# Performance work log

Hardware: AMD Instinct MI355X
Metric: run time of the kernel (lower is better)

## Reference

```python
import jax, jax.numpy as jnp
import numpy as np

H = 768; P = 128; HEADS = 12; LAYERS = 3; T = 17; VD = 10
D = H // HEADS
H2 = H // 2


def _ln(x, s, b, eps=1e-5):
    m = x.mean(-1, keepdims=True)
    v = ((x - m) ** 2).mean(-1, keepdims=True)
    return (x - m) * jax.lax.rsqrt(v + eps) * s + b


def _gru_dir(x, wih, whh, bih, bhh, reverse):
    # torch nn.GRU single direction, batch_first
    if reverse:
        x = x[:, ::-1]
    xw = x @ wih.T + bih  # [B,N,3*H2]
    def step(h, xw_t):
        gh = h @ whh.T + bhh
        ir, iz, inn = jnp.split(xw_t, 3, -1)
        hr, hz, hn = jnp.split(gh, 3, -1)
        r = jax.nn.sigmoid(ir + hr)
        z = jax.nn.sigmoid(iz + hz)
        n = jnp.tanh(inn + r * hn)
        h = (1.0 - z) * n + z * h
        return h, h
    h0 = jnp.zeros((x.shape[0], whh.shape[1]), x.dtype)
    _, ys = jax.lax.scan(step, h0, jnp.swapaxes(xw, 0, 1))
    ys = jnp.swapaxes(ys, 0, 1)
    return ys[:, ::-1] if reverse else ys


def setup_inputs():
    B, EDU = 2, 95
    N = EDU + 1
    key = jax.random.key(0)
    ks = iter(jax.random.split(key, 64))
    def nrm(shape, s=0.02):
        return s * jax.random.normal(next(ks), shape, jnp.float32)
    inp = {}
    inp['sentences'] = jax.random.normal(next(ks), (B, EDU, H), jnp.float32)
    inp['speakers'] = jax.random.randint(next(ks), (B, N, N), 0, 2)
    inp['turns'] = jax.random.randint(next(ks), (B, N, N), 0, 2)
    g = jax.random.randint(next(ks), (B, N, N), 0, T)
    inp['graphs'] = jnp.tril(g, -1)  # gold graph: lower-triangular relation labels
    inp['edu_nums'] = jax.random.randint(next(ks), (B,), 60, N + 1)
    inp['root'] = jnp.zeros((H,), jnp.float32)
    for d_ in ['f', 'b']:
        inp[f'gru_wih_{d_}'] = nrm((3 * H2, H))
        inp[f'gru_whh_{d_}'] = nrm((3 * H2, H2))
        inp[f'gru_bih_{d_}'] = jnp.zeros((3 * H2,), jnp.float32)
        inp[f'gru_bhh_{d_}'] = jnp.zeros((3 * H2,), jnp.float32)
    inp['emb_speaker'] = nrm((2, P // 4), 1.0)
    inp['emb_turn'] = nrm((2, P // 4), 1.0)
    inp['emb_position'] = nrm((2 * VD + 3, P // 2), 1.0)
    inp['normal_type'] = nrm((T - 1, P), P ** -0.5)
    inp['wr'] = nrm((P, 2 * H + P)); inp['br'] = jnp.zeros((P,), jnp.float32)
    inp['wz'] = nrm((P, 2 * H + P)); inp['bz'] = jnp.zeros((P,), jnp.float32)
    inp['wc'] = nrm((P, 2 * H)); inp['bc'] = jnp.zeros((P,), jnp.float32)
    inp['wu'] = nrm((P, P)); inp['bu'] = jnp.zeros((P,), jnp.float32)
    for nm in ['wq', 'wk', 'wv', 'wo']:
        inp[nm] = nrm((H, H))
    for nm in ['bq', 'bk', 'bv', 'bo']:
        inp[nm] = jnp.zeros((H,), jnp.float32)
    inp['wsk'] = nrm((D, P)); inp['bsk'] = jnp.zeros((D,), jnp.float32)
    inp['wsv'] = nrm((D, P)); inp['bsv'] = jnp.zeros((D,), jnp.float32)
    inp['ln_s'] = jnp.ones((H,), jnp.float32); inp['ln_b'] = jnp.zeros((H,), jnp.float32)
    inp['pln_s'] = jnp.ones((P,), jnp.float32); inp['pln_b'] = jnp.zeros((P,), jnp.float32)
    CIN = 4 * H + P
    inp['link_w1'] = nrm((H, CIN)); inp['link_b1'] = jnp.zeros((H,), jnp.float32)
    inp['link_w2'] = nrm((1, H)); inp['link_b2'] = jnp.zeros((1,), jnp.float32)
    inp['lab_w1'] = nrm((H, CIN)); inp['lab_b1'] = jnp.zeros((H,), jnp.float32)
    inp['lab_w2'] = nrm((T, H)); inp['lab_b2'] = jnp.zeros((T,), jnp.float32)
    return inp


def reference(sentences, speakers, turns, graphs, edu_nums, root,
              gru_wih_f, gru_whh_f, gru_bih_f, gru_bhh_f,
              gru_wih_b, gru_whh_b, gru_bih_b, gru_bhh_b,
              emb_speaker, emb_turn, emb_position, normal_type,
              wr, br, wz, bz, wc, bc, wu, bu,
              wq, bq, wk, bk, wv, bv, wo, bo, wsk, bsk, wsv, bsv,
              ln_s, ln_b, pln_s, pln_b,
              link_w1, link_b1, link_w2, link_b2,
              lab_w1, lab_b1, lab_w2, lab_b2):
    B, EDU, _ = sentences.shape
    N = EDU + 1
    # root node + EDU embeddings -> bidirectional dialog GRU
    dialog_input = jnp.concatenate([jnp.broadcast_to(root, (B, 1, H)), sentences], axis=1)
    fw = _gru_dir(dialog_input, gru_wih_f, gru_whh_f, gru_bih_f, gru_bhh_f, False)
    bw = _gru_dir(dialog_input, gru_wih_b, gru_whh_b, gru_bih_b, gru_bhh_b, True)
    dialog_output = jnp.concatenate([fw, bw], -1)  # [B,N,H]
    # attention masking bias
    valid = jnp.arange(N)[None, :] < edu_nums[:, None]
    bias = jnp.where(valid, 0.0, -1e9)[:, None, None, :]  # [B,1,1,N]
    # constant path embedding (speaker / turn / relative position)
    idx = jnp.arange(N)
    rel = jnp.clip(idx[None, :] - idx[:, None], -VD - 1, VD + 1) + VD + 1
    pos = jnp.broadcast_to(emb_position[rel][None], (B, N, N, P // 2))
    const_path = jnp.concatenate([emb_speaker[speakers], emb_turn[turns], pos], -1)
    # gold structure path from relation labels (PathModel, padding_idx=0)
    labels = jnp.concatenate([jnp.zeros((1, P), normal_type.dtype), normal_type], 0)
    struct_path = labels[graphs + jnp.swapaxes(graphs, 1, 2)]  # [B,N,N,P]
    tril = jnp.tril(jnp.ones((N, N), bool), -1)
    triu = jnp.triu(jnp.ones((N, N), bool), 1)
    nodes = dialog_output
    scale = D ** -0.5
    for _ in range(LAYERS):
        # dns2ds: symmetrize (in-place in torch, so struct_path is replaced)
        struct_path = jnp.where(triu[None, :, :, None], jnp.swapaxes(struct_path, 1, 2), struct_path)
        paths = _ln(struct_path + const_path, pln_s, pln_b)
        q = (nodes @ wq.T + bq).reshape(B, N, HEADS, D).transpose(0, 2, 1, 3) * scale
        k = (nodes @ wk.T + bk).reshape(B, N, HEADS, D).transpose(0, 2, 1, 3)
        v = (nodes @ wv.T + bv).reshape(B, N, HEADS, D).transpose(0, 2, 1, 3)
        sk = paths @ wsk.T + bsk  # [B,N,N,D]
        sv = paths @ wsv.T + bsv
        w = (jnp.einsum('bhnd,bhmd->bhnm', q, k)
             + jnp.einsum('bhnd,bnmd->bhnm', q, sk) + bias)
        w = jax.nn.softmax(w, -1)
        out = (jnp.einsum('bhnm,bhmd->bhnd', w, v)
               + jnp.einsum('bhnm,bnmd->bhnd', w, sv))
        out = out.transpose(0, 2, 1, 3).reshape(B, N, H)
        nodes = _ln(nodes + jax.nn.relu(out @ wo.T + bo), ln_s, ln_b)
        # PathUpdateModel (GRU-style update on lower-triangular pairs)
        a = jnp.broadcast_to(nodes[:, None, :, :], (B, N, N, H))  # a[b,i,j]=nodes[b,j]
        pair = jnp.concatenate([a, jnp.swapaxes(a, 1, 2)], -1)  # [B,N,N,2H]
        rz = jnp.concatenate([pair, struct_path], -1)
        r = jax.nn.sigmoid(rz @ wr.T + br)
        z = jax.nn.sigmoid(rz @ wz.T + bz)
        u = jnp.tanh(pair @ wc.T + bc + r * (struct_path @ wu.T + bu))
        new = z * struct_path + (1.0 - z) * u
        struct_path = jnp.where(tril[None, :, :, None], new, struct_path)
    # pairwise classifier features
    multi = jnp.concatenate([dialog_input, dialog_output], -1)  # [B,N,2H]
    e = jnp.broadcast_to(multi[:, None, :, :], (B, N, N, 2 * H))
    feats = jnp.concatenate([e, jnp.swapaxes(e, 1, 2), struct_path], -1)  # [B,N,N,4H+P]
    link = (jnp.tanh(feats @ link_w1.T + link_b1) @ link_w2.T + link_b2)[..., 0]
    label = jnp.tanh(feats @ lab_w1.T + lab_b1) @ lab_w2.T + lab_b2
    return (link, label)
```

## Files before the change

kernel.cpp:

```cpp
#include <hip/hip_runtime.h>
#include <math.h>

typedef unsigned short u16;
typedef short bf16x8 __attribute__((ext_vector_type(8)));
typedef float f32x4 __attribute__((ext_vector_type(4)));


static constexpr size_t O_MULTI  = 0;
static constexpr size_t O_XWF    = O_MULTI + 294912;
static constexpr size_t O_XWB    = O_XWF   + 221184;
static constexpr size_t O_HBUF   = O_XWB   + 221184;
static constexpr size_t O_CONST  = O_HBUF  + 3072;
static constexpr size_t O_STRUCT = O_CONST + 2359296;
static constexpr size_t O_PATHS  = O_STRUCT+ 2359296;
static constexpr size_t O_NODES  = O_PATHS + 2359296;
static constexpr size_t O_QB     = O_NODES + 147456;
static constexpr size_t O_KB     = O_QB    + 147456;
static constexpr size_t O_VB     = O_KB    + 147456;
static constexpr size_t O_SKB    = O_VB    + 147456;
static constexpr size_t O_SVB    = O_SKB   + 1179648;
static constexpr size_t O_ATT    = O_SVB   + 1179648;
static constexpr size_t O_NP     = O_ATT   + 147456;
static constexpr size_t O_LAL    = O_NP    + 147456;
static constexpr size_t O_LBL    = O_LAL   + 147456;
static constexpr size_t O_LAB    = O_LBL   + 147456;
static constexpr size_t O_LBB    = O_LAB   + 147456;
static constexpr size_t O_END    = O_LBB   + 147456;

static constexpr int B_QW  = 0;
static constexpr int B_KW  = 589824;
static constexpr int B_VW  = 1179648;
static constexpr int B_OW  = 1769472;
static constexpr int B_IHF = 2359296;
static constexpr int B_IHB = 3244032;
static constexpr int B_RA  = 4128768;
static constexpr int B_RB  = 4227072;
static constexpr int B_ZA  = 4325376;
static constexpr int B_ZB  = 4423680;
static constexpr int B_CA  = 4521984;
static constexpr int B_CB  = 4620288;
static constexpr int B_CBF = 4718592;
static constexpr int B_MBF = 4980736;
static constexpr int B_NBF = 5275648;
static constexpr int B_ABF = 5423104;
static constexpr int B_TOT = 5570560;
static constexpr int CVT_TOT = 4980736;

static constexpr int C_WSK = 0;
static constexpr int C_WSV = 8192;
static constexpr int C_WRS = 16384;
static constexpr int C_WZS = 32768;
static constexpr int C_WU  = 49152;
static constexpr int C_W1L = 65536;
static constexpr int C_W1B = 163840;

__device__ __forceinline__ u16 f2bf(float f) {
  union { float f; unsigned u; } v; v.f = f;
  unsigned r = v.u + 0x7fff + ((v.u >> 16) & 1);
  return (u16)(r >> 16);
}

__global__ void init_kernel(const float* __restrict__ sentences,
                            const float* __restrict__ root,
                            float* __restrict__ multi, u16* __restrict__ multibf,
                            int* bar) {
  int idx = blockIdx.x * 256 + threadIdx.x;
  if (idx < 12) bar[idx * 64] = 0;
  if (idx >= 2 * 96 * 768) return;
  int c = idx % 768;
  int rem = idx / 768;
  int t = rem % 96;
  int b = rem / 96;
  float v = (t == 0) ? root[c] : sentences[((size_t)(b * 95 + (t - 1))) * 768 + c];
  size_t a = ((size_t)(b * 96 + t)) * 1536 + c;
  multi[a] = v;
  multibf[a] = f2bf(v);
}

__global__ void init_pairs_kernel(const int* __restrict__ speakers,
                                  const int* __restrict__ turns,
                                  const int* __restrict__ graphs,
                                  const float* __restrict__ emb_speaker,
                                  const float* __restrict__ emb_turn,
                                  const float* __restrict__ emb_position,
                                  const float* __restrict__ normal_type,
                                  float* __restrict__ cpath,
                                  float* __restrict__ spath) {
  int idx = blockIdx.x * 256 + threadIdx.x;
  if (idx >= 18432 * 128) return;
  int c = idx & 127;
  int p = idx >> 7;
  int j = p % 96;
  int rem = p / 96;
  int i = rem % 96;
  int b = rem / 96;
  float cv;
  if (c < 32) {
    cv = emb_speaker[speakers[p] * 32 + c];
  } else if (c < 64) {
    cv = emb_turn[turns[p] * 32 + (c - 32)];
  } else {
    int d = j - i;
    d = min(max(d, -11), 11) + 11;
    cv = emb_position[d * 64 + (c - 64)];
  }
  cpath[idx] = cv;
  int g2 = graphs[p] + graphs[(b * 96 + j) * 96 + i];
  spath[idx] = (g2 == 0) ? 0.f : normal_type[(g2 - 1) * 128 + c];
}

__global__ void cvt_weights_kernel(const float* __restrict__ wq, const float* __restrict__ wk,
                                   const float* __restrict__ wv, const float* __restrict__ wo,
                                   const float* __restrict__ wih_f, const float* __restrict__ wih_b,
                                   const float* __restrict__ wr, const float* __restrict__ wz,
                                   const float* __restrict__ wc, const float* __restrict__ wsk,
                                   const float* __restrict__ wsv, const float* __restrict__ wu,
                                   const float* __restrict__ link_w1, const float* __restrict__ lab_w1,
                                   u16* __restrict__ wbf) {
  int idx = blockIdx.x * 256 + threadIdx.x;
  if (idx >= CVT_TOT) return;
  float v;
  if (idx < B_IHF) {
    int which = idx / 589824, r = idx % 589824;
    const float* src = which == 0 ? wq : which == 1 ? wk : which == 2 ? wv : wo;
    v = src[r];
  } else if (idx < B_RA) {
    int r = idx - B_IHF;
    v = (r < 884736) ? wih_f[r] : wih_b[r - 884736];
  } else if (idx < B_CBF) {
    int r = idx - B_RA;
    int seg = r / 98304, q = r % 98304;
    int row = q / 768, c = q % 768;
    switch (seg) {
      case 0: v = wr[(size_t)row * 1664 + c]; break;
      case 1: v = wr[(size_t)row * 1664 + 768 + c]; break;
      case 2: v = wz[(size_t)row * 1664 + c]; break;
      case 3: v = wz[(size_t)row * 1664 + 768 + c]; break;
      case 4: v = wc[(size_t)row * 1536 + c]; break;
      default: v = wc[(size_t)row * 1536 + 768 + c]; break;
    }
  } else {
    int r = idx - B_CBF;
    if (r < C_WSV) v = wsk[r];
    else if (r < C_WRS) v = wsv[r - C_WSV];
    else if (r < C_WZS) { int q = r - C_WRS; v = wr[(size_t)(q >> 7) * 1664 + 1536 + (q & 127)]; }
    else if (r < C_WU)  { int q = r - C_WZS; v = wz[(size_t)(q >> 7) * 1664 + 1536 + (q & 127)]; }
    else if (r < C_W1L) v = wu[r - C_WU];
    else if (r < C_W1B) { int q = r - C_W1L; v = link_w1[(size_t)(q >> 7) * 3200 + 3072 + (q & 127)]; }
    else { int q = r - C_W1B; v = lab_w1[(size_t)(q >> 7) * 3200 + 3072 + (q & 127)]; }
  }
  wbf[idx] = f2bf(v);
}

__global__ void cvt_w1ab_kernel(const float* __restrict__ link_w1,
                                const float* __restrict__ lab_w1,
                                u16* __restrict__ l1, u16* __restrict__ b1) {
  int idx = blockIdx.x * 256 + threadIdx.x;
  if (idx >= 2359296) return;
  int half = idx / 1179648;
  int r = idx % 1179648;
  int row = r / 1536, c = r % 1536;
  size_t src = (size_t)row * 3200 + half * 1536 + c;
  l1[idx] = f2bf(link_w1[src]);
  b1[idx] = f2bf(lab_w1[src]);
}

struct BJob { const u16* W; const float* bias; float* C; };
struct BJobs { BJob j[6]; };

__global__ __launch_bounds__(256) void bgemm_kernel(const u16* __restrict__ A,
                                                    int lda, int K, int N, BJobs jobs) {
  BJob jb = jobs.j[blockIdx.z];
  int r0 = blockIdx.x * 16;
  int tid = threadIdx.x;
  int wave = tid >> 6, lane = tid & 63;
  int col = lane & 15, quad = lane >> 4;
  int c = blockIdx.y * 64 + wave * 16 + col;
  const u16* arow = A + (size_t)(r0 + col) * lda + quad * 8;
  const u16* brow = jb.W + (size_t)c * K + quad * 8;
  f32x4 acc = {0.f, 0.f, 0.f, 0.f};
  for (int k = 0; k < K; k += 32) {
    bf16x8 af = *(const bf16x8*)(arow + k);
    bf16x8 bf = *(const bf16x8*)(brow + k);
    acc = __builtin_amdgcn_mfma_f32_16x16x32_bf16(af, bf, acc, 0, 0, 0);
  }
  float bv = jb.bias ? jb.bias[c] : 0.f;
#pragma unroll
  for (int r = 0; r < 4; ++r)
    jb.C[(size_t)(r0 + quad * 4 + r) * N + c] = acc[r] + bv;
}

__global__ __launch_bounds__(512) void gru_kernel(const float* __restrict__ whh_f,
                                                  const float* __restrict__ whh_b,
                                                  const float* __restrict__ bhh_f,
                                                  const float* __restrict__ bhh_b,
                                                  const float* __restrict__ xwf,
                                                  const float* __restrict__ xwb,
                                                  float* hbuf, float* multi,
                                                  u16* multibf, int* bar) {
  int dir = blockIdx.x / 6;
  int sub = blockIdx.x % 6;
  const float* whh = dir ? whh_b : whh_f;
  const float* bhh = dir ? bhh_b : bhh_f;
  const float* xw = dir ? xwb : xwf;
  float* hb = hbuf + (size_t)dir * 1536;
  int* flags = bar + dir * 6 * 64;

  __shared__ float hlds[768];
  __shared__ float part[3][64][2][17];

  int tid = threadIdx.x;
  int ks = tid >> 5;
  int ug = tid & 31;
  int hv0 = ug * 2;

  float4 wreg[6][6];
#pragma unroll
  for (int d = 0; d < 2; ++d)
#pragma unroll
    for (int g = 0; g < 3; ++g) {
      const float* wrow = whh + (size_t)(g * 384 + sub * 64 + hv0 + d) * 384 + ks * 24;
#pragma unroll
      for (int m = 0; m < 6; ++m) wreg[d * 3 + g][m] = *(const float4*)(wrow + m * 4);
    }
  float bh0 = 0.f, bh1 = 0.f, bh2 = 0.f;
  int hvC = 0, bsel = 0;
  if (tid < 128) {
    hvC = sub * 64 + (tid >> 1);
    bsel = tid & 1;
    bh0 = bhh[hvC];
    bh1 = bhh[384 + hvC];
    bh2 = bhh[768 + hvC];
  }

  for (int s = 0; s < 96; ++s) {
    int t = dir ? (95 - s) : s;
    float xr = 0.f, xz = 0.f, xn = 0.f;
    if (tid < 128) {
      const float* xrow = xw + (size_t)(bsel * 96 + t) * 1152;
      xr = xrow[hvC]; xz = xrow[384 + hvC]; xn = xrow[768 + hvC];
    }
    if (s == 0) {
      __syncthreads();
      for (int k = tid; k < 768; k += 512) hlds[k] = 0.f;
    } else {
      if (tid < 6) {
        while (__hip_atomic_load(&flags[tid * 64], __ATOMIC_RELAXED,
                                 __HIP_MEMORY_SCOPE_AGENT) < s)
          __builtin_amdgcn_s_sleep(1);
      }
      __syncthreads();
      const float* hsrc = hb + ((s - 1) & 1) * 768;
      for (int k = tid; k < 768; k += 512)
        hlds[k] = __hip_atomic_load(&hsrc[k], __ATOMIC_RELAXED, __HIP_MEMORY_SCOPE_AGENT);
    }
    __syncthreads();

    float acc[6][2];
#pragma unroll
    for (int b = 0; b < 2; ++b) {
      float4 h4[6];
      const float* hp = hlds + b * 384 + ks * 24;
#pragma unroll
      for (int m = 0; m < 6; ++m) h4[m] = *(const float4*)(hp + m * 4);
#pragma unroll
      for (int u = 0; u < 6; ++u) {
        float ssum = 0.f;
#pragma unroll
        for (int m = 0; m < 6; ++m) {
          float4 w = wreg[u][m];
          ssum += w.x * h4[m].x + w.y * h4[m].y + w.z * h4[m].z + w.w * h4[m].w;
        }
        acc[u][b] = ssum;
      }
    }
#pragma unroll
    for (int d = 0; d < 2; ++d)
#pragma unroll
      for (int g = 0; g < 3; ++g) {
        part[g][hv0 + d][0][ks] = acc[d * 3 + g][0];
        part[g][hv0 + d][1][ks] = acc[d * 3 + g][1];
      }
    __syncthreads();

    float hn = 0.f;
    if (tid < 128) {
      int hv = tid >> 1;
      float gr = bh0, gz = bh1, gn = bh2;
#pragma unroll
      for (int q = 0; q < 16; ++q) {
        gr += part[0][hv][bsel][q];
        gz += part[1][hv][bsel][q];
        gn += part[2][hv][bsel][q];
      }
      float r = 1.f / (1.f + expf(-(xr + gr)));
      float z = 1.f / (1.f + expf(-(xz + gz)));
      float n = tanhf(xn + r * gn);
      float hp = hlds[bsel * 384 + hvC];
      hn = (1.f - z) * n + z * hp;
      __hip_atomic_store(&hb[(s & 1) * 768 + bsel * 384 + hvC], hn, __ATOMIC_RELAXED,
                         __HIP_MEMORY_SCOPE_AGENT);
    }
    asm volatile("s_waitcnt vmcnt(0)" ::: "memory");
    __syncthreads();
    if (tid == 0)
      __hip_atomic_store(&flags[sub * 64], s + 1, __ATOMIC_RELAXED,
                         __HIP_MEMORY_SCOPE_AGENT);
    if (tid < 128) {
      size_t a = ((size_t)(bsel * 96 + t)) * 1536 + 768 + dir * 384 + hvC;
      multi[a] = hn;
      multibf[a] = f2bf(hn);
    }
  }
}

__global__ __launch_bounds__(256) void ln_paths_kernel(float* __restrict__ spath,
                                                       const float* __restrict__ cpath,
                                                       const float* __restrict__ pln_s,
                                                       const float* __restrict__ pln_b,
                                                       u16* __restrict__ paths) {
  int p = blockIdx.x * 4 + (threadIdx.x >> 6);
  int lane = threadIdx.x & 63;
  int j = p % 96;
  int rem = p / 96;
  int i = rem % 96;
  int b = rem / 96;
  size_t self = (size_t)p * 128;
  const float* src = (i < j) ? (spath + ((size_t)((b * 96 + j) * 96 + i)) * 128)
                             : (spath + self);
  float v0 = src[lane], v1 = src[lane + 64];
  if (i < j) {
    spath[self + lane] = v0;
    spath[self + lane + 64] = v1;
  }
  float x0 = v0 + cpath[self + lane];
  float x1 = v1 + cpath[self + lane + 64];
  float s = x0 + x1;
  for (int off = 32; off; off >>= 1) s += __shfl_xor(s, off, 64);
  float mean = s * (1.f / 128.f);
  float d0 = x0 - mean, d1 = x1 - mean;
  float vs = d0 * d0 + d1 * d1;
  for (int off = 32; off; off >>= 1) vs += __shfl_xor(vs, off, 64);
  float rstd = rsqrtf(vs * (1.f / 128.f) + 1e-5f);
  paths[self + lane] = f2bf(d0 * rstd * pln_s[lane] + pln_b[lane]);
  paths[self + lane + 64] = f2bf(d1 * rstd * pln_s[lane + 64] + pln_b[lane + 64]);
}

__global__ __launch_bounds__(256) void sksv_mfma_kernel(const u16* __restrict__ paths,
                                                        const u16* __restrict__ cbf,
                                                        const float* __restrict__ bsk,
                                                        const float* __restrict__ bsv,
                                                        float* __restrict__ skb,
                                                        float* __restrict__ svb) {
  const u16* wb = cbf + (blockIdx.y ? C_WSV : C_WSK);
  const float* bias = blockIdx.y ? bsv : bsk;
  float* out = blockIdx.y ? svb : skb;
  int p0 = blockIdx.x * 64;
  int tid = threadIdx.x;
  int wave = tid >> 6, lane = tid & 63;
  int col = lane & 15, quad = lane >> 4;

  bf16x8 afrag[4];
  const u16* arow = paths + (size_t)(p0 + wave * 16 + col) * 128 + quad * 8;
#pragma unroll
  for (int c = 0; c < 4; ++c) afrag[c] = *(const bf16x8*)(arow + 32 * c);

#pragma unroll
  for (int nt = 0; nt < 4; ++nt) {
    f32x4 acc = {0.f, 0.f, 0.f, 0.f};
    const u16* brow = wb + (size_t)(nt * 16 + col) * 128 + quad * 8;
#pragma unroll
    for (int c = 0; c < 4; ++c) {
      bf16x8 bf = *(const bf16x8*)(brow + 32 * c);
      acc = __builtin_amdgcn_mfma_f32_16x16x32_bf16(afrag[c], bf, acc, 0, 0, 0);
    }
    int o = nt * 16 + col;
    float bv = bias[o];
#pragma unroll
    for (int r = 0; r < 4; ++r)
      out[(size_t)(p0 + wave * 16 + quad * 4 + r) * 64 + o] = acc[r] + bv;
  }
}

__global__ __launch_bounds__(256) void attn_kernel(const float* __restrict__ qb,
                                                   const float* __restrict__ kb,
                                                   const float* __restrict__ vb,
                                                   const float* __restrict__ skb,
                                                   const float* __restrict__ svb,
                                                   const int* __restrict__ edu_nums,
                                                   u16* __restrict__ attout) {
  int bi = blockIdx.x;
  int b = bi / 96;
  __shared__ float qrow[768];
  __shared__ float sc[12][100];
  int tid = threadIdx.x;
  for (int k = tid; k < 768; k += 256) qrow[k] = qb[(size_t)bi * 768 + k];
  int edun = edu_nums[b];
  __syncthreads();
  for (int task = tid; task < 12 * 96; task += 256) {
    int h = task / 96, j = task % 96;
    const float* krow = kb + ((size_t)(b * 96 + j)) * 768 + h * 64;
    const float* skrow = skb + ((size_t)(bi * 96 + j)) * 64;
    float s = 0.f;
    for (int d4 = 0; d4 < 64; d4 += 4) {
      float4 qv = *(const float4*)(qrow + h * 64 + d4);
      float4 kv = *(const float4*)(krow + d4);
      float4 sv = *(const float4*)(skrow + d4);
      s += qv.x * (kv.x + sv.x) + qv.y * (kv.y + sv.y) + qv.z * (kv.z + sv.z) +
           qv.w * (kv.w + sv.w);
    }
    s *= 0.125f;
    if (j >= edun) s -= 1e9f;
    sc[h][j] = s;
  }
  __syncthreads();
  if (tid < 12) {
    int h = tid;
    float m = -3.4e38f;
    for (int j = 0; j < 96; ++j) m = fmaxf(m, sc[h][j]);
    float sum = 0.f;
    for (int j = 0; j < 96; ++j) {
      float e = expf(sc[h][j] - m);
      sc[h][j] = e;
      sum += e;
    }
    float r = 1.f / sum;
    for (int j = 0; j < 96; ++j) sc[h][j] *= r;
  }
  __syncthreads();
  for (int o = tid; o < 768; o += 256) {
    int h = o >> 6, d = o & 63;
    float acc = 0.f;
    const float* vcol = vb + (size_t)(b * 96) * 768 + o;
    const float* svcol = svb + ((size_t)(bi * 96)) * 64 + d;
    for (int j = 0; j < 96; ++j) acc += sc[h][j] * (vcol[j * 768] + svcol[j * 64]);
    attout[(size_t)bi * 768 + o] = f2bf(acc);
  }
}

__global__ __launch_bounds__(256) void ln_nodes_kernel(const float* __restrict__ src,
                                                       int lda,
                                                       const float* __restrict__ proj,
                                                       const float* __restrict__ ln_s,
                                                       const float* __restrict__ ln_b,
                                                       float* __restrict__ nodes,
                                                       u16* __restrict__ nodesbf) {
  int row = blockIdx.x * 4 + (threadIdx.x >> 6);
  int lane = threadIdx.x & 63;
  float x[12];
  float s = 0.f;
#pragma unroll
  for (int m = 0; m < 12; ++m) {
    int e = lane + m * 64;
    float v = src[(size_t)row * lda + e] + fmaxf(proj[(size_t)row * 768 + e], 0.f);
    x[m] = v;
    s += v;
  }
  for (int off = 32; off; off >>= 1) s += __shfl_xor(s, off, 64);
  float mean = s * (1.f / 768.f);
  float vs = 0.f;
#pragma unroll
  for (int m = 0; m < 12; ++m) {
    float d = x[m] - mean;
    x[m] = d;
    vs += d * d;
  }
  for (int off = 32; off; off >>= 1) vs += __shfl_xor(vs, off, 64);
  float rstd = rsqrtf(vs * (1.f / 768.f) + 1e-5f);
#pragma unroll
  for (int m = 0; m < 12; ++m) {
    int e = lane + m * 64;
    float v = x[m] * rstd * ln_s[e] + ln_b[e];
    nodes[(size_t)row * 768 + e] = v;
    nodesbf[(size_t)row * 768 + e] = f2bf(v);
  }
}

__global__ __launch_bounds__(256) void gate_mfma_kernel(float* __restrict__ spath,
                                                        const float* __restrict__ np,
                                                        const u16* __restrict__ cbf,
                                                        const float* __restrict__ br,
                                                        const float* __restrict__ bz,
                                                        const float* __restrict__ bc,
                                                        const float* __restrict__ bu) {
  __shared__ int addrs[16], npi[16], npj[16];
  int tid = threadIdx.x;
  if (tid < 16) {
    int pid = blockIdx.x * 16 + tid;
    int b = pid / 4560;
    int t = pid % 4560;
    int i = (int)((sqrtf(8.f * (float)t + 1.f) + 1.f) * 0.5f);
    while (i * (i - 1) / 2 > t) --i;
    while ((i + 1) * i / 2 <= t) ++i;
    int j = t - i * (i - 1) / 2;
    addrs[tid] = ((b * 96 + i) * 96 + j) * 128;
    npi[tid] = (b * 96 + i) * 128;
    npj[tid] = (b * 96 + j) * 128;
  }
  __syncthreads();

  int wave = tid >> 6, lane = tid & 63;
  int col = lane & 15, quad = lane >> 4;

  bf16x8 afrag[4];
  {
    const float* arow = spath + (size_t)addrs[col] + quad * 8;
#pragma unroll
    for (int c = 0; c < 4; ++c) {
      bf16x8 f;
#pragma unroll
      for (int q = 0; q < 8; ++q) f[q] = (short)f2bf(arow[32 * c + q]);
      afrag[c] = f;
    }
  }

  const u16* wrs = cbf + C_WRS;
  const u16* wzs = cbf + C_WZS;
  const u16* wu = cbf + C_WU;

  f32x4 cr[2], cz[2], cu[2];
#pragma unroll
  for (int ct = 0; ct < 2; ++ct) {
    cr[ct] = {0.f, 0.f, 0.f, 0.f};
    cz[ct] = {0.f, 0.f, 0.f, 0.f};
    cu[ct] = {0.f, 0.f, 0.f, 0.f};
    int o0 = wave * 32 + ct * 16;
    const u16* br_ = wrs + (size_t)(o0 + col) * 128 + quad * 8;
    const u16* bz_ = wzs + (size_t)(o0 + col) * 128 + quad * 8;
    const u16* bu_ = wu + (size_t)(o0 + col) * 128 + quad * 8;
#pragma unroll
    for (int c = 0; c < 4; ++c) {
      cr[ct] = __builtin_amdgcn_mfma_f32_16x16x32_bf16(afrag[c], *(const bf16x8*)(br_ + 32 * c), cr[ct], 0, 0, 0);
      cz[ct] = __builtin_amdgcn_mfma_f32_16x16x32_bf16(afrag[c], *(const bf16x8*)(bz_ + 32 * c), cz[ct], 0, 0, 0);
      cu[ct] = __builtin_amdgcn_mfma_f32_16x16x32_bf16(afrag[c], *(const bf16x8*)(bu_ + 32 * c), cu[ct], 0, 0, 0);
    }
  }

#pragma unroll
  for (int ct = 0; ct < 2; ++ct) {
    int o = wave * 32 + ct * 16 + col;
    float brv = br[o], bzv = bz[o], bcv = bc[o], buv = bu[o];
#pragma unroll
    for (int r4 = 0; r4 < 4; ++r4) {
      int m = quad * 4 + r4;
      int sa = addrs[m] + o;
      float so = spath[sa];
      float nra = np[0 * 24576 + npj[m] + o];
      float nrb = np[1 * 24576 + npi[m] + o];
      float nza = np[2 * 24576 + npj[m] + o];
      float nzb = np[3 * 24576 + npi[m] + o];
      float nca = np[4 * 24576 + npj[m] + o];
      float ncb = np[5 * 24576 + npi[m] + o];
      float r = 1.f / (1.f + expf(-(cr[ct][r4] + nra + nrb + brv)));
      float z = 1.f / (1.f + expf(-(cz[ct][r4] + nza + nzb + bzv)));
      float u = tanhf(nca + ncb + bcv + r * (cu[ct][r4] + buv));
      spath[sa] = z * so + (1.f - z) * u;
    }
  }
}

__global__ void cvt_spath_kernel(const float* __restrict__ sp, u16* __restrict__ out) {
  int idx = blockIdx.x * 256 + threadIdx.x;
  float4 v = *(const float4*)(sp + (size_t)idx * 4);
  u16* o = out + (size_t)idx * 4;
  o[0] = f2bf(v.x); o[1] = f2bf(v.y); o[2] = f2bf(v.z); o[3] = f2bf(v.w);
}

__global__ __launch_bounds__(256) void final_mfma_kernel(
    const u16* __restrict__ spbf, const u16* __restrict__ cbf,
    const float* __restrict__ LAl, const float* __restrict__ LBl,
    const float* __restrict__ LAb, const float* __restrict__ LBb,
    const float* __restrict__ w2l, const float* __restrict__ w2b,
    const float* __restrict__ b2l, const float* __restrict__ b2b,
    float* __restrict__ outlink, float* __restrict__ outlab) {
  const u16* w1l = cbf + C_W1L;
  const u16* w1b = cbf + C_W1B;
  int p0 = blockIdx.x * 16;
  int j0 = p0 % 96;
  int rem = p0 / 96;
  int i = rem % 96;
  int b = rem / 96;
  int tid = threadIdx.x;
  int wave = tid >> 6;
  int lane = tid & 63;
  int col = lane & 15;
  int quad = lane >> 4;

  __shared__ float redl[4][16];
  __shared__ float red[4][16][17];

  bf16x8 afrag[4];
  {
    const u16* arow = spbf + (size_t)(p0 + col) * 128 + quad * 8;
#pragma unroll
    for (int c = 0; c < 4; ++c) afrag[c] = *(const bf16x8*)(arow + 32 * c);
  }

  float lacc[4] = {0.f, 0.f, 0.f, 0.f};
  float at[4][17];
#pragma unroll
  for (int r = 0; r < 4; ++r)
#pragma unroll
    for (int t = 0; t < 17; ++t) at[r][t] = 0.f;

  const float* LBl_row = LBl + (size_t)(b * 96 + i) * 768;
  const float* LBb_row = LBb + (size_t)(b * 96 + i) * 768;

  for (int nt = wave; nt < 48; nt += 4) {
    int o0 = nt * 16;
    f32x4 c = {0.f, 0.f, 0.f, 0.f};
    const u16* brow = w1l + (size_t)(o0 + col) * 128 + quad * 8;
#pragma unroll
    for (int cc = 0; cc < 4; ++cc) {
      bf16x8 bf = *(const bf16x8*)(brow + 32 * cc);
      c = __builtin_amdgcn_mfma_f32_16x16x32_bf16(afrag[cc], bf, c, 0, 0, 0);
    }
    int o = o0 + col;
    float lb = LBl_row[o];
    float w2 = w2l[o];
#pragma unroll
    for (int r = 0; r < 4; ++r) {
      int m = quad * 4 + r;
      float la = LAl[(size_t)(b * 96 + j0 + m) * 768 + o];
      float h = tanhf(c[r] + la + lb);
      lacc[r] += h * w2;
    }
  }

  for (int nt = wave; nt < 48; nt += 4) {
    int o0 = nt * 16;
    f32x4 c = {0.f, 0.f, 0.f, 0.f};
    const u16* brow = w1b + (size_t)(o0 + col) * 128 + quad * 8;
#pragma unroll
    for (int cc = 0; cc < 4; ++cc) {
      bf16x8 bf = *(const bf16x8*)(brow + 32 * cc);
      c = __builtin_amdgcn_mfma_f32_16x16x32_bf16(afrag[cc], bf, c, 0, 0, 0);
    }
    int o = o0 + col;
    float lb = LBb_row[o];
#pragma unroll
    for (int r = 0; r < 4; ++r) {
      int m = quad * 4 + r;
      float la = LAb[(size_t)(b * 96 + j0 + m) * 768 + o];
      float h = tanhf(c[r] + la + lb);
#pragma unroll
      for (int t = 0; t < 17; ++t) at[r][t] += h * w2b[t * 768 + o];
    }
  }

#pragma unroll
  for (int r = 0; r < 4; ++r) {
    lacc[r] += __shfl_xor(lacc[r], 1, 64);
    lacc[r] += __shfl_xor(lacc[r], 2, 64);
    lacc[r] += __shfl_xor(lacc[r], 4, 64);
    lacc[r] += __shfl_xor(lacc[r], 8, 64);
#pragma unroll
    for (int t = 0; t < 17; ++t) {
      at[r][t] += __shfl_xor(at[r][t], 1, 64);
      at[r][t] += __shfl_xor(at[r][t], 2, 64);
      at[r][t] += __shfl_xor(at[r][t], 4, 64);
      at[r][t] += __shfl_xor(at[r][t], 8, 64);
    }
  }
  if (col == 0) {
#pragma unroll
    for (int r = 0; r < 4; ++r) {
      int m = quad * 4 + r;
      redl[wave][m] = lacc[r];
#pragma unroll
      for (int t = 0; t < 17; ++t) red[wave][m][t] = at[r][t];
    }
  }
  __syncthreads();
  if (tid < 16) {
    float s = redl[0][tid] + redl[1][tid] + redl[2][tid] + redl[3][tid];
    outlink[(size_t)((b * 96 + i) * 96) + j0 + tid] = s + b2l[0];
  }
  for (int task = tid; task < 16 * 17; task += 256) {
    int m = task / 17, t = task % 17;
    float s = red[0][m][t] + red[1][m][t] + red[2][m][t] + red[3][m][t];
    outlab[((size_t)((b * 96 + i) * 96) + j0 + m) * 17 + t] = s + b2b[t];
  }
}

extern "C" void kernel_launch(void* const* d_in, const int* in_sizes, int n_in,
                              void* d_out, int out_size, void* d_ws, size_t ws_size,
                              hipStream_t stream) {
  (void)in_sizes; (void)n_in; (void)out_size; (void)ws_size;
  const float* sentences = (const float*)d_in[0];
  const int* speakers = (const int*)d_in[1];
  const int* turns = (const int*)d_in[2];
  const int* graphs = (const int*)d_in[3];
  const int* edu_nums = (const int*)d_in[4];
  const float* root = (const float*)d_in[5];
  const float* wih_f = (const float*)d_in[6];
  const float* whh_f = (const float*)d_in[7];
  const float* bih_f = (const float*)d_in[8];
  const float* bhh_f = (const float*)d_in[9];
  const float* wih_b = (const float*)d_in[10];
  const float* whh_b = (const float*)d_in[11];
  const float* bih_b = (const float*)d_in[12];
  const float* bhh_b = (const float*)d_in[13];
  const float* emb_speaker = (const float*)d_in[14];
  const float* emb_turn = (const float*)d_in[15];
  const float* emb_position = (const float*)d_in[16];
  const float* normal_type = (const float*)d_in[17];
  const float* wr = (const float*)d_in[18];
  const float* br = (const float*)d_in[19];
  const float* wz = (const float*)d_in[20];
  const float* bz = (const float*)d_in[21];
  const float* wc = (const float*)d_in[22];
  const float* bc = (const float*)d_in[23];
  const float* wu = (const float*)d_in[24];
  const float* bu = (const float*)d_in[25];
  const float* wq = (const float*)d_in[26];
  const float* wk = (const float*)d_in[27];
  const float* wv = (const float*)d_in[28];
  const float* wo = (const float*)d_in[29];
  const float* bq = (const float*)d_in[30];
  const float* bk = (const float*)d_in[31];
  const float* bv = (const float*)d_in[32];
  const float* bo = (const float*)d_in[33];
  const float* wsk = (const float*)d_in[34];
  const float* bsk = (const float*)d_in[35];
  const float* wsv = (const float*)d_in[36];
  const float* bsv = (const float*)d_in[37];
  const float* ln_s = (const float*)d_in[38];
  const float* ln_b = (const float*)d_in[39];
  const float* pln_s = (const float*)d_in[40];
  const float* pln_b = (const float*)d_in[41];
  const float* link_w1 = (const float*)d_in[42];
  const float* link_b1 = (const float*)d_in[43];
  const float* link_w2 = (const float*)d_in[44];
  const float* link_b2 = (const float*)d_in[45];
  const float* lab_w1 = (const float*)d_in[46];
  const float* lab_b1 = (const float*)d_in[47];
  const float* lab_w2 = (const float*)d_in[48];
  const float* lab_b2 = (const float*)d_in[49];

  int* bar = (int*)d_ws;
  float* W = (float*)((char*)d_ws + 4096);
  float* multi = W + O_MULTI;
  float* xwf = W + O_XWF;
  float* xwb = W + O_XWB;
  float* hbuf = W + O_HBUF;
  float* cpath = W + O_CONST;
  float* spath = W + O_STRUCT;
  float* nodes = W + O_NODES;
  float* qb = W + O_QB;
  float* kb = W + O_KB;
  float* vb = W + O_VB;
  float* skb = W + O_SKB;
  float* svb = W + O_SVB;
  float* np = W + O_NP;
  float* LAl = W + O_LAL;
  float* LBl = W + O_LBL;
  float* LAb = W + O_LAB;
  float* LBb = W + O_LBB;
  u16* pathsbf = (u16*)(W + O_PATHS);
  u16* wbf = (u16*)(W + O_END);
  u16* cbf = wbf + B_CBF;
  u16* multibf = wbf + B_MBF;
  u16* nodesbf = wbf + B_NBF;
  u16* attoutbf = wbf + B_ABF;
  float* outlink = (float*)d_out;
  float* outlab = (float*)d_out + 18432;

  init_kernel<<<576, 256, 0, stream>>>(sentences, root, multi, multibf, bar);

  cvt_weights_kernel<<<19456, 256, 0, stream>>>(wq, wk, wv, wo, wih_f, wih_b, wr, wz,
                                                wc, wsk, wsv, wu, link_w1, lab_w1, wbf);

  {
    BJobs j{};
    j.j[0] = {wbf + B_IHF, bih_f, xwf};
    j.j[1] = {wbf + B_IHB, bih_b, xwb};
    bgemm_kernel<<<dim3(12, 18, 2), 256, 0, stream>>>(multibf, 1536, 768, 1152, j);
  }

  init_pairs_kernel<<<9216, 256, 0, stream>>>(speakers, turns, graphs, emb_speaker,
                                              emb_turn, emb_position, normal_type,
                                              cpath, spath);

  gru_kernel<<<12, 512, 0, stream>>>(whh_f, whh_b, bhh_f, bhh_b, xwf, xwb, hbuf,
                                     multi, multibf, bar);

  for (int layer = 0; layer < 3; ++layer) {
    const u16* nsrcbf = (layer == 0) ? (multibf + 768) : nodesbf;
    int nlda = (layer == 0) ? 1536 : 768;
    const float* nsrc = (layer == 0) ? (multi + 768) : nodes;

    ln_paths_kernel<<<4608, 256, 0, stream>>>(spath, cpath, pln_s, pln_b, pathsbf);

    {
      BJobs j{};
      j.j[0] = {wbf + B_QW, bq, qb};
      j.j[1] = {wbf + B_KW, bk, kb};
      j.j[2] = {wbf + B_VW, bv, vb};
      bgemm_kernel<<<dim3(12, 12, 3), 256, 0, stream>>>(nsrcbf, nlda, 768, 768, j);
    }

    sksv_mfma_kernel<<<dim3(288, 2), 256, 0, stream>>>(pathsbf, cbf, bsk, bsv, skb,
                                                       svb);

    attn_kernel<<<192, 256, 0, stream>>>(qb, kb, vb, skb, svb, edu_nums, attoutbf);

    {
      BJobs j{};
      j.j[0] = {wbf + B_OW, bo, qb};
      bgemm_kernel<<<dim3(12, 12, 1), 256, 0, stream>>>(attoutbf, 768, 768, 768, j);
    }

    ln_nodes_kernel<<<48, 256, 0, stream>>>(nsrc, nlda, qb, ln_s, ln_b, nodes,
                                            nodesbf);

    {
      BJobs j{};
      j.j[0] = {wbf + B_RA, nullptr, np + 0 * 24576};
      j.j[1] = {wbf + B_RB, nullptr, np + 1 * 24576};
      j.j[2] = {wbf + B_ZA, nullptr, np + 2 * 24576};
      j.j[3] = {wbf + B_ZB, nullptr, np + 3 * 24576};
      j.j[4] = {wbf + B_CA, nullptr, np + 4 * 24576};
      j.j[5] = {wbf + B_CB, nullptr, np + 5 * 24576};
      bgemm_kernel<<<dim3(12, 2, 6), 256, 0, stream>>>(nodesbf, 768, 768, 128, j);
    }

    gate_mfma_kernel<<<570, 256, 0, stream>>>(spath, np, cbf, br, bz, bc, bu);
  }

  cvt_spath_kernel<<<2304, 256, 0, stream>>>(spath, pathsbf);

  u16* l1 = (u16*)skb;
  u16* b1 = (u16*)svb;
  cvt_w1ab_kernel<<<9216, 256, 0, stream>>>(link_w1, lab_w1, l1, b1);

  {
    BJobs j{};
    j.j[0] = {l1, link_b1, LAl};
    j.j[1] = {l1 + 1179648, nullptr, LBl};
    j.j[2] = {b1, lab_b1, LAb};
    j.j[3] = {b1 + 1179648, nullptr, LBb};
    bgemm_kernel<<<dim3(12, 12, 4), 256, 0, stream>>>(multibf, 1536, 1536, 768, j);
  }

  final_mfma_kernel<<<1152, 256, 0, stream>>>(pathsbf, cbf, LAl, LBl, LAb, LBb,
                                              link_w2, lab_w2, link_b2, lab_b2,
                                              outlink, outlab);
}
```

Measured before the change: 1.004 ms.

## Overlap path LN/sk-sv and weight conversion with GRU in one kernel; fuse out-proj with LN

The sequential GRU kernel, which uses only 12 blocks, now launches extra blocks. These run the layer-0 path layernorm plus sk/sv projection and the link/label W1 bf16 conversion on otherwise idle CUs, in parallel with the recurrence. The path LN and the sk/sv MFMA are fused into one kernel that stages normalised rows in LDS, so the bf16 paths buffer is no longer written and read back. The output projection is fused with the residual layernorm, and the final kernel converts spath to bf16 on the fly, dropping the separate conversion kernels. Risks: the GRU blocks rely on spin flags, so co-resident extra blocks could delay them, and oln uses only 12 blocks.

```diff
diff --git a/kernel.cpp b/kernel.cpp
--- a/kernel.cpp
+++ b/kernel.cpp
@@ -43,7 +43,6 @@
 static constexpr int B_MBF = 4980736;
 static constexpr int B_NBF = 5275648;
 static constexpr int B_ABF = 5423104;
-static constexpr int B_TOT = 5570560;
 static constexpr int CVT_TOT = 4980736;
 
 static constexpr int C_WSK = 0;
@@ -152,19 +151,6 @@
   wbf[idx] = f2bf(v);
 }
 
-__global__ void cvt_w1ab_kernel(const float* __restrict__ link_w1,
-                                const float* __restrict__ lab_w1,
-                                u16* __restrict__ l1, u16* __restrict__ b1) {
-  int idx = blockIdx.x * 256 + threadIdx.x;
-  if (idx >= 2359296) return;
-  int half = idx / 1179648;
-  int r = idx % 1179648;
-  int row = r / 1536, c = r % 1536;
-  size_t src = (size_t)row * 3200 + half * 1536 + c;
-  l1[idx] = f2bf(link_w1[src]);
-  b1[idx] = f2bf(lab_w1[src]);
-}
-
 struct BJob { const u16* W; const float* bias; float* C; };
 struct BJobs { BJob j[6]; };
 
@@ -190,26 +176,131 @@
     jb.C[(size_t)(r0 + quad * 4 + r) * N + c] = acc[r] + bv;
 }
 
-__global__ __launch_bounds__(512) void gru_kernel(const float* __restrict__ whh_f,
-                                                  const float* __restrict__ whh_b,
-                                                  const float* __restrict__ bhh_f,
-                                                  const float* __restrict__ bhh_b,
-                                                  const float* __restrict__ xwf,
-                                                  const float* __restrict__ xwb,
-                                                  float* hbuf, float* multi,
-                                                  u16* multibf, int* bar) {
-  int dir = blockIdx.x / 6;
-  int sub = blockIdx.x % 6;
+__device__ __forceinline__ void lnsksv_body(int blk, int tid,
+                                            float* __restrict__ spath,
+                                            const float* __restrict__ cpath,
+                                            const float* __restrict__ pln_s,
+                                            const float* __restrict__ pln_b,
+                                            const u16* __restrict__ cbf,
+                                            const float* __restrict__ bsk,
+                                            const float* __restrict__ bsv,
+                                            float* __restrict__ skb,
+                                            float* __restrict__ svb,
+                                            int store_upper, u16* plds) {
+  int p0 = blk * 64;
+  int wave = tid >> 6, lane = tid & 63;
+  float pls0 = pln_s[lane], pls1 = pln_s[lane + 64];
+  float plb0 = pln_b[lane], plb1 = pln_b[lane + 64];
+#pragma unroll
+  for (int pp = 0; pp < 8; ++pp) {
+    int pl = wave * 8 + pp;
+    int p = p0 + pl;
+    int j = p % 96;
+    int rem = p / 96;
+    int i = rem % 96;
+    int b = rem / 96;
+    size_t self = (size_t)p * 128;
+    const float* src = (i < j) ? (spath + ((size_t)((b * 96 + j) * 96 + i)) * 128)
+                               : (spath + self);
+    float v0 = src[lane], v1 = src[lane + 64];
+    if (store_upper && i < j) {
+      spath[self + lane] = v0;
+      spath[self + lane + 64] = v1;
+    }
+    float x0 = v0 + cpath[self + lane];
+    float x1 = v1 + cpath[self + lane + 64];
+    float s = x0 + x1;
+    for (int off = 32; off; off >>= 1) s += __shfl_xor(s, off, 64);
+    float mean = s * (1.f / 128.f);
+    float d0 = x0 - mean, d1 = x1 - mean;
+    float vs = d0 * d0 + d1 * d1;
+    for (int off = 32; off; off >>= 1) vs += __shfl_xor(vs, off, 64);
+    float rstd = rsqrtf(vs * (1.f / 128.f) + 1e-5f);
+    plds[pl * 136 + lane] = f2bf(d0 * rstd * pls0 + plb0);
+    plds[pl * 136 + lane + 64] = f2bf(d1 * rstd * pls1 + plb1);
+  }
+  __syncthreads();
+  int mat = wave >> 2, rowg = wave & 3;
+  const u16* wb = cbf + (mat ? C_WSV : C_WSK);
+  const float* bias = mat ? bsv : bsk;
+  float* out = mat ? svb : skb;
+  int col = lane & 15, quad = lane >> 4;
+  bf16x8 afrag[4];
+  const u16* arow = plds + (rowg * 16 + col) * 136 + quad * 8;
+#pragma unroll
+  for (int c = 0; c < 4; ++c) afrag[c] = *(const bf16x8*)(arow + 32 * c);
+#pragma unroll
+  for (int nt = 0; nt < 4; ++nt) {
+    f32x4 acc = {0.f, 0.f, 0.f, 0.f};
+    const u16* brow = wb + (size_t)(nt * 16 + col) * 128 + quad * 8;
+#pragma unroll
+    for (int c = 0; c < 4; ++c)
+      acc = __builtin_amdgcn_mfma_f32_16x16x32_bf16(afrag[c], *(const bf16x8*)(brow + 32 * c), acc, 0, 0, 0);
+    int o = nt * 16 + col;
+    float bv = bias[o];
+#pragma unroll
+    for (int r = 0; r < 4; ++r)
+      out[(size_t)(p0 + rowg * 16 + quad * 4 + r) * 64 + o] = acc[r] + bv;
+  }
+}
+
+__global__ __launch_bounds__(512) void lnsksv_kernel(float* __restrict__ spath,
+                                                     const float* __restrict__ cpath,
+                                                     const float* __restrict__ pln_s,
+                                                     const float* __restrict__ pln_b,
+                                                     const u16* __restrict__ cbf,
+                                                     const float* __restrict__ bsk,
+                                                     const float* __restrict__ bsv,
+                                                     float* __restrict__ skb,
+                                                     float* __restrict__ svb,
+                                                     int store_upper) {
+  __shared__ u16 plds[64 * 136];
+  lnsksv_body(blockIdx.x, threadIdx.x, spath, cpath, pln_s, pln_b, cbf, bsk, bsv,
+              skb, svb, store_upper, plds);
+}
+
+__global__ __launch_bounds__(512) void mega_gru_kernel(
+    const float* __restrict__ whh_f, const float* __restrict__ whh_b,
+    const float* __restrict__ bhh_f, const float* __restrict__ bhh_b,
+    const float* __restrict__ xwf, const float* __restrict__ xwb,
+    float* hbuf, float* multi, u16* multibf, int* bar,
+    float* __restrict__ spath, const float* __restrict__ cpath,
+    const float* __restrict__ pln_s, const float* __restrict__ pln_b,
+    const u16* __restrict__ cbf, const float* __restrict__ bsk,
+    const float* __restrict__ bsv, float* __restrict__ skb,
+    float* __restrict__ svb, const float* __restrict__ link_w1,
+    const float* __restrict__ lab_w1, u16* __restrict__ l1, u16* __restrict__ b1) {
+  __shared__ float hlds[768];
+  __shared__ float part[3][64][2][17];
+  __shared__ u16 plds[64 * 136];
+  int bx = blockIdx.x;
+  int tid = threadIdx.x;
+
+  if (bx >= 300) {
+    for (int idx = (bx - 300) * 512 + tid; idx < 2359296; idx += 84 * 512) {
+      int half = idx / 1179648;
+      int r = idx % 1179648;
+      int row = r / 1536, c = r % 1536;
+      size_t src = (size_t)row * 3200 + half * 1536 + c;
+      l1[idx] = f2bf(link_w1[src]);
+      b1[idx] = f2bf(lab_w1[src]);
+    }
+    return;
+  }
+  if (bx >= 12) {
+    lnsksv_body(bx - 12, tid, spath, cpath, pln_s, pln_b, cbf, bsk, bsv, skb, svb,
+                0, plds);
+    return;
+  }
+
+  int dir = bx / 6;
+  int sub = bx % 6;
   const float* whh = dir ? whh_b : whh_f;
   const float* bhh = dir ? bhh_b : bhh_f;
   const float* xw = dir ? xwb : xwf;
   float* hb = hbuf + (size_t)dir * 1536;
   int* flags = bar + dir * 6 * 64;
 
-  __shared__ float hlds[768];
-  __shared__ float part[3][64][2][17];
-
-  int tid = threadIdx.x;
   int ks = tid >> 5;
   int ug = tid & 31;
   int hv0 = ug * 2;
@@ -311,74 +402,6 @@
       multi[a] = hn;
       multibf[a] = f2bf(hn);
     }
-  }
-}
-
-__global__ __launch_bounds__(256) void ln_paths_kernel(float* __restrict__ spath,
-                                                       const float* __restrict__ cpath,
-                                                       const float* __restrict__ pln_s,
-                                                       const float* __restrict__ pln_b,
-                                                       u16* __restrict__ paths) {
-  int p = blockIdx.x * 4 + (threadIdx.x >> 6);
-  int lane = threadIdx.x & 63;
-  int j = p % 96;
-  int rem = p / 96;
-  int i = rem % 96;
-  int b = rem / 96;
-  size_t self = (size_t)p * 128;
-  const float* src = (i < j) ? (spath + ((size_t)((b * 96 + j) * 96 + i)) * 128)
-                             : (spath + self);
-  float v0 = src[lane], v1 = src[lane + 64];
-  if (i < j) {
-    spath[self + lane] = v0;
-    spath[self + lane + 64] = v1;
-  }
-  float x0 = v0 + cpath[self + lane];
-  float x1 = v1 + cpath[self + lane + 64];
-  float s = x0 + x1;
-  for (int off = 32; off; off >>= 1) s += __shfl_xor(s, off, 64);
-  float mean = s * (1.f / 128.f);
-  float d0 = x0 - mean, d1 = x1 - mean;
-  float vs = d0 * d0 + d1 * d1;
-  for (int off = 32; off; off >>= 1) vs += __shfl_xor(vs, off, 64);
-  float rstd = rsqrtf(vs * (1.f / 128.f) + 1e-5f);
-  paths[self + lane] = f2bf(d0 * rstd * pln_s[lane] + pln_b[lane]);
-  paths[self + lane + 64] = f2bf(d1 * rstd * pln_s[lane + 64] + pln_b[lane + 64]);
-}
-
-__global__ __launch_bounds__(256) void sksv_mfma_kernel(const u16* __restrict__ paths,
-                                                        const u16* __restrict__ cbf,
-                                                        const float* __restrict__ bsk,
-                                                        const float* __restrict__ bsv,
-                                                        float* __restrict__ skb,
-                                                        float* __restrict__ svb) {
-  const u16* wb = cbf + (blockIdx.y ? C_WSV : C_WSK);
-  const float* bias = blockIdx.y ? bsv : bsk;
-  float* out = blockIdx.y ? svb : skb;
-  int p0 = blockIdx.x * 64;
-  int tid = threadIdx.x;
-  int wave = tid >> 6, lane = tid & 63;
-  int col = lane & 15, quad = lane >> 4;
-
-  bf16x8 afrag[4];
-  const u16* arow = paths + (size_t)(p0 + wave * 16 + col) * 128 + quad * 8;
-#pragma unroll
-  for (int c = 0; c < 4; ++c) afrag[c] = *(const bf16x8*)(arow + 32 * c);
-
-#pragma unroll
-  for (int nt = 0; nt < 4; ++nt) {
-    f32x4 acc = {0.f, 0.f, 0.f, 0.f};
-    const u16* brow = wb + (size_t)(nt * 16 + col) * 128 + quad * 8;
-#pragma unroll
-    for (int c = 0; c < 4; ++c) {
-      bf16x8 bf = *(const bf16x8*)(brow + 32 * c);
-      acc = __builtin_amdgcn_mfma_f32_16x16x32_bf16(afrag[c], bf, acc, 0, 0, 0);
-    }
-    int o = nt * 16 + col;
-    float bv = bias[o];
-#pragma unroll
-    for (int r = 0; r < 4; ++r)
-      out[(size_t)(p0 + wave * 16 + quad * 4 + r) * 64 + o] = acc[r] + bv;
   }
 }
 
@@ -438,41 +461,71 @@
   }
 }
 
-__global__ __launch_bounds__(256) void ln_nodes_kernel(const float* __restrict__ src,
-                                                       int lda,
-                                                       const float* __restrict__ proj,
-                                                       const float* __restrict__ ln_s,
-                                                       const float* __restrict__ ln_b,
-                                                       float* __restrict__ nodes,
-                                                       u16* __restrict__ nodesbf) {
-  int row = blockIdx.x * 4 + (threadIdx.x >> 6);
-  int lane = threadIdx.x & 63;
-  float x[12];
-  float s = 0.f;
-#pragma unroll
-  for (int m = 0; m < 12; ++m) {
-    int e = lane + m * 64;
-    float v = src[(size_t)row * lda + e] + fmaxf(proj[(size_t)row * 768 + e], 0.f);
-    x[m] = v;
-    s += v;
-  }
-  for (int off = 32; off; off >>= 1) s += __shfl_xor(s, off, 64);
-  float mean = s * (1.f / 768.f);
-  float vs = 0.f;
-#pragma unroll
-  for (int m = 0; m < 12; ++m) {
-    float d = x[m] - mean;
-    x[m] = d;
-    vs += d * d;
-  }
-  for (int off = 32; off; off >>= 1) vs += __shfl_xor(vs, off, 64);
-  float rstd = rsqrtf(vs * (1.f / 768.f) + 1e-5f);
-#pragma unroll
-  for (int m = 0; m < 12; ++m) {
-    int e = lane + m * 64;
-    float v = x[m] * rstd * ln_s[e] + ln_b[e];
-    nodes[(size_t)row * 768 + e] = v;
-    nodesbf[(size_t)row * 768 + e] = f2bf(v);
+__global__ __launch_bounds__(256) void oln_kernel(const u16* __restrict__ attoutbf,
+                                                  const u16* __restrict__ wo_bf,
+                                                  const float* __restrict__ bo,
+                                                  const float* __restrict__ src,
+                                                  int lda,
+                                                  const float* __restrict__ ln_s,
+                                                  const float* __restrict__ ln_b,
+                                                  float* __restrict__ nodes,
+                                                  u16* __restrict__ nodesbf) {
+  __shared__ float buf[16][772];
+  int r0 = blockIdx.x * 16;
+  int tid = threadIdx.x;
+  int wave = tid >> 6, lane = tid & 63;
+  int col = lane & 15, quad = lane >> 4;
+
+  bf16x8 af[24];
+  const u16* arow = attoutbf + (size_t)(r0 + col) * 768 + quad * 8;
+#pragma unroll
+  for (int c = 0; c < 24; ++c) af[c] = *(const bf16x8*)(arow + 32 * c);
+
+  for (int nt = wave; nt < 48; nt += 4) {
+    int o0 = nt * 16;
+    f32x4 acc = {0.f, 0.f, 0.f, 0.f};
+    const u16* brow = wo_bf + (size_t)(o0 + col) * 768 + quad * 8;
+#pragma unroll
+    for (int c = 0; c < 24; ++c)
+      acc = __builtin_amdgcn_mfma_f32_16x16x32_bf16(af[c], *(const bf16x8*)(brow + 32 * c), acc, 0, 0, 0);
+    int o = o0 + col;
+    float bv = bo[o];
+#pragma unroll
+    for (int r = 0; r < 4; ++r) {
+      int row = quad * 4 + r;
+      buf[row][o] = src[(size_t)(r0 + row) * lda + o] + fmaxf(acc[r] + bv, 0.f);
+    }
+  }
+  __syncthreads();
+
+#pragma unroll
+  for (int rr = 0; rr < 4; ++rr) {
+    int row = wave * 4 + rr;
+    float x[12];
+    float s = 0.f;
+#pragma unroll
+    for (int m = 0; m < 12; ++m) {
+      x[m] = buf[row][lane + m * 64];
+      s += x[m];
+    }
+    for (int off = 32; off; off >>= 1) s += __shfl_xor(s, off, 64);
+    float mean = s * (1.f / 768.f);
+    float vs = 0.f;
+#pragma unroll
+    for (int m = 0; m < 12; ++m) {
+      float d = x[m] - mean;
+      x[m] = d;
+      vs += d * d;
+    }
+    for (int off = 32; off; off >>= 1) vs += __shfl_xor(vs, off, 64);
+    float rstd = rsqrtf(vs * (1.f / 768.f) + 1e-5f);
+#pragma unroll
+    for (int m = 0; m < 12; ++m) {
+      int e = lane + m * 64;
+      float v = x[m] * rstd * ln_s[e] + ln_b[e];
+      nodes[(size_t)(r0 + row) * 768 + e] = v;
+      nodesbf[(size_t)(r0 + row) * 768 + e] = f2bf(v);
+    }
   }
 }
 
@@ -559,15 +612,8 @@
   }
 }
 
-__global__ void cvt_spath_kernel(const float* __restrict__ sp, u16* __restrict__ out) {
-  int idx = blockIdx.x * 256 + threadIdx.x;
-  float4 v = *(const float4*)(sp + (size_t)idx * 4);
-  u16* o = out + (size_t)idx * 4;
-  o[0] = f2bf(v.x); o[1] = f2bf(v.y); o[2] = f2bf(v.z); o[3] = f2bf(v.w);
-}
-
 __global__ __launch_bounds__(256) void final_mfma_kernel(
-    const u16* __restrict__ spbf, const u16* __restrict__ cbf,
+    const float* __restrict__ spath, const u16* __restrict__ cbf,
     const float* __restrict__ LAl, const float* __restrict__ LBl,
     const float* __restrict__ LAb, const float* __restrict__ LBb,
     const float* __restrict__ w2l, const float* __restrict__ w2b,
@@ -591,9 +637,14 @@
 
   bf16x8 afrag[4];
   {
-    const u16* arow = spbf + (size_t)(p0 + col) * 128 + quad * 8;
-#pragma unroll
-    for (int c = 0; c < 4; ++c) afrag[c] = *(const bf16x8*)(arow + 32 * c);
+    const float* arow = spath + (size_t)(p0 + col) * 128 + quad * 8;
+#pragma unroll
+    for (int c = 0; c < 4; ++c) {
+      bf16x8 f;
+#pragma unroll
+      for (int q = 0; q < 8; ++q) f[q] = (short)f2bf(arow[32 * c + q]);
+      afrag[c] = f;
+    }
   }
 
   float lacc[4] = {0.f, 0.f, 0.f, 0.f};
@@ -757,7 +808,8 @@
   float* LBl = W + O_LBL;
   float* LAb = W + O_LAB;
   float* LBb = W + O_LBB;
-  u16* pathsbf = (u16*)(W + O_PATHS);
+  u16* l1 = (u16*)(W + O_PATHS);
+  u16* b1 = l1 + 2359296;
   u16* wbf = (u16*)(W + O_END);
   u16* cbf = wbf + B_CBF;
   u16* multibf = wbf + B_MBF;
@@ -782,15 +834,19 @@
                                               emb_turn, emb_position, normal_type,
                                               cpath, spath);
 
-  gru_kernel<<<12, 512, 0, stream>>>(whh_f, whh_b, bhh_f, bhh_b, xwf, xwb, hbuf,
-                                     multi, multibf, bar);
+  mega_gru_kernel<<<384, 512, 0, stream>>>(whh_f, whh_b, bhh_f, bhh_b, xwf, xwb,
+                                           hbuf, multi, multibf, bar, spath, cpath,
+                                           pln_s, pln_b, cbf, bsk, bsv, skb, svb,
+                                           link_w1, lab_w1, l1, b1);
 
   for (int layer = 0; layer < 3; ++layer) {
     const u16* nsrcbf = (layer == 0) ? (multibf + 768) : nodesbf;
     int nlda = (layer == 0) ? 1536 : 768;
     const float* nsrc = (layer == 0) ? (multi + 768) : nodes;
 
-    ln_paths_kernel<<<4608, 256, 0, stream>>>(spath, cpath, pln_s, pln_b, pathsbf);
+    if (layer > 0)
+      lnsksv_kernel<<<288, 512, 0, stream>>>(spath, cpath, pln_s, pln_b, cbf, bsk,
+                                             bsv, skb, svb, layer == 2 ? 1 : 0);
 
     {
       BJobs j{};
@@ -800,19 +856,10 @@
       bgemm_kernel<<<dim3(12, 12, 3), 256, 0, stream>>>(nsrcbf, nlda, 768, 768, j);
     }
 
-    sksv_mfma_kernel<<<dim3(288, 2), 256, 0, stream>>>(pathsbf, cbf, bsk, bsv, skb,
-                                                       svb);
-
     attn_kernel<<<192, 256, 0, stream>>>(qb, kb, vb, skb, svb, edu_nums, attoutbf);
 
-    {
-      BJobs j{};
-      j.j[0] = {wbf + B_OW, bo, qb};
-      bgemm_kernel<<<dim3(12, 12, 1), 256, 0, stream>>>(attoutbf, 768, 768, 768, j);
-    }
-
-    ln_nodes_kernel<<<48, 256, 0, stream>>>(nsrc, nlda, qb, ln_s, ln_b, nodes,
-                                            nodesbf);
+    oln_kernel<<<12, 256, 0, stream>>>(attoutbf, wbf + B_OW, bo, nsrc, nlda, ln_s,
+                                       ln_b, nodes, nodesbf);
 
     {
       BJobs j{};
@@ -828,12 +875,6 @@
     gate_mfma_kernel<<<570, 256, 0, stream>>>(spath, np, cbf, br, bz, bc, bu);
   }
 
-  cvt_spath_kernel<<<2304, 256, 0, stream>>>(spath, pathsbf);
-
-  u16* l1 = (u16*)skb;
-  u16* b1 = (u16*)svb;
-  cvt_w1ab_kernel<<<9216, 256, 0, stream>>>(link_w1, lab_w1, l1, b1);
-
   {
     BJobs j{};
     j.j[0] = {l1, link_b1, LAl};
@@ -843,7 +884,7 @@
     bgemm_kernel<<<dim3(12, 12, 4), 256, 0, stream>>>(multibf, 1536, 1536, 768, j);
   }
 
-  final_mfma_kernel<<<1152, 256, 0, stream>>>(pathsbf, cbf, LAl, LBl, LAb, LBb,
+  final_mfma_kernel<<<1152, 256, 0, stream>>>(spath, cbf, LAl, LBl, LAb, LBb,
                                               link_w2, lab_w2, link_b2, lab_b2,
                                               outlink, outlab);
 }
```

After: 1.086 ms. +8.2%, slower.
